# Optimization experiments

Measured on AMD Instinct MI355X. Metric: run time of the kernel, lower is better.

Reference implementation:

```python
import jax, jax.numpy as jnp
import numpy as np

H = 128          # hidden_size
B = 64           # batch of users
T = 20           # current-session length (== max_sess_len)
S = 10           # friend sessions per user (graph degree)
L = 20           # max_sess_len
NUM_ITEMS = 50000
NUM_USERS = 10000
TOPK = 2         # topk in sess_similarity


def gru(x, W_ih, W_hh, b_ih, b_hh):
    """torch nn.GRU (1 layer, batch_first). x: [N, T, H] -> outputs [N, T, H], h_T [N, H]."""
    h0 = jnp.zeros((x.shape[0], x.shape[-1]), x.dtype)

    def step(h, xt):
        gi = xt @ W_ih.T + b_ih          # [N, 3H]
        gh = h @ W_hh.T + b_hh
        i_r, i_z, i_n = jnp.split(gi, 3, axis=-1)
        h_r, h_z, h_n = jnp.split(gh, 3, axis=-1)
        r = jax.nn.sigmoid(i_r + h_r)
        z = jax.nn.sigmoid(i_z + h_z)
        n = jnp.tanh(i_n + r * h_n)
        h = (1.0 - z) * n + z * h
        return h, h

    hT, ys = jax.lax.scan(step, h0, jnp.swapaxes(x, 0, 1))
    return jnp.swapaxes(ys, 0, 1), hT


def masked_softmax(x, mask, axis):
    neg = jnp.finfo(x.dtype).min
    return jax.nn.softmax(jnp.where(mask, x, neg), axis=axis)


def setup_inputs() -> dict:
    key = jax.random.key(0)
    ks = jax.random.split(key, 12)
    users = jax.random.randint(ks[0], (B,), 0, NUM_USERS)
    cur_sess = jax.random.randint(ks[1], (B, T), 0, NUM_ITEMS)          # all valid -> full length
    hist_sess = jax.random.randint(ks[2], (B, S, L), 0, NUM_ITEMS)
    frds_sess = jax.random.randint(ks[3], (B, S, L), 0, NUM_ITEMS)
    cur_sess_len = jnp.full((B,), T, dtype=jnp.int32)
    # parameters
    v_emb = jax.random.uniform(ks[4], (NUM_ITEMS + 1, H), minval=-1.0, maxval=1.0)
    v_emb = v_emb.at[NUM_ITEMS].set(0.0)                                 # padding_idx row
    u_emb = jax.random.normal(ks[5], (NUM_USERS, H)) * (1.0 / np.sqrt(H))
    sc = 1.0 / np.sqrt(H)
    W_ih = jax.random.normal(ks[6], (3 * H, H)) * sc
    W_hh = jax.random.normal(ks[7], (3 * H, H)) * sc
    b_ih = jnp.zeros((3 * H,), jnp.float32)
    b_hh = jnp.zeros((3 * H,), jnp.float32)
    out1_w = jax.random.normal(ks[8], (NUM_ITEMS, 3 * H)) * (1.0 / np.sqrt(3 * H))
    out1_b = jnp.zeros((NUM_ITEMS,), jnp.float32)
    return dict(users=users, cur_sess=cur_sess, hist_sess=hist_sess, frds_sess=frds_sess,
                cur_sess_len=cur_sess_len, v_emb=v_emb, u_emb=u_emb,
                W_ih=W_ih, W_hh=W_hh, b_ih=b_ih, b_hh=b_hh, out1_w=out1_w, out1_b=out1_b)


def reference(users, cur_sess, hist_sess, frds_sess, cur_sess_len,
              v_emb, u_emb, W_ih, W_hh, b_ih, b_hh, out1_w, out1_b):
    # --- rnn_encoder on current session (dropout p=0, eval) ---
    hs, _ = gru(v_emb[cur_sess], W_ih, W_hh, b_ih, b_hh)                 # [B, T, H]
    query = hs

    # --- friend branch (hist branch is dead: hu is overwritten with zeros) ---
    # sess_encoder: GRU over each friend session's items
    frd_items = v_emb[frds_sess]                                         # [B, S, L, H]
    enc, _ = gru(frd_items.reshape(B * S, L, H), W_ih, W_hh, b_ih, b_hh)
    enc = enc.reshape(B, S, L, H)                                        # encoder_output

    # sess_similarity: max over session positions, softmax over degree (S)
    scores = jnp.einsum('bth,bslh->bstl', query, enc)                    # [B, S, T, L]
    sim_raw = scores.max(axis=-1)                                        # [B, S, T]
    sim1 = jax.nn.softmax(sim_raw, axis=1)
    # preserve: edges that are top-2 most similar for ANY step t (S > TOPK branch)
    _, idx = jax.lax.top_k(jnp.swapaxes(sim1, 1, 2), TOPK)               # [B, T, 2]
    preserve = jax.nn.one_hot(idx, S, dtype=jnp.float32).sum((1, 2)) > 0 # [B, S]

    # sess_embedding_attn on the filtered subgraph (masking == filtering here)
    user_e = u_emb[users]                                                # [B, H]
    w = jax.nn.softmax(jnp.einsum('bh,bslh->bsl', user_e, frd_items), axis=2)
    sess_emb = jnp.einsum('bsl,bslh->bsh', w, frd_items)                 # [B, S, H]

    # user_sess_reduce_func: sim1 (pre-filter softmax values), then two softmaxes
    # over the surviving edges (masked softmax over S)
    m = preserve[:, :, None]                                             # [B, S, 1]
    s = masked_softmax(sim1, m, axis=1)
    s = masked_softmax(s, m, axis=1)
    s = jnp.where(m, s, 0.0)
    hf = jnp.einsum('bst,bsh->bth', s, sess_emb)                         # [B, T, H]

    hu = jnp.zeros_like(hs)                                              # hu = zeros_like(hs)
    output = jnp.concatenate([hs, hu, hf], axis=-1)                      # [B, T, 3H]
    logits = output @ out1_w.T + out1_b                                  # [B, T, NUM_ITEMS]
    return logits
```

## Files before the change

### kernel.cpp

```cpp
#include <hip/hip_runtime.h>
#include <cstdint>
#include <cstddef>

#define H_      128
#define B_      64
#define T_      20
#define S_      10
#define L_      20
#define NITEMS  50000
#define NSEQ    704
#define NTOK    (NSEQ * 20)
#define NPAD    50048
#define KA      256

typedef __attribute__((ext_vector_type(8))) short short8;
typedef __attribute__((ext_vector_type(4))) float f32x4;

__device__ __forceinline__ unsigned short f2bf(float f) {
  unsigned int u = __float_as_uint(f);
  u += 0x7FFF + ((u >> 16) & 1);
  return (unsigned short)(u >> 16);
}
__device__ __forceinline__ float sigmoidf_(float x) {
  return 1.0f / (1.0f + __expf(-x));
}

__global__ void __launch_bounds__(384) k2_gi(const int* __restrict__ cur,
                                             const int* __restrict__ frd,
                                             const float* __restrict__ vemb,
                                             const float* __restrict__ Wih,
                                             const float* __restrict__ bih,
                                             float* __restrict__ gi) {
  __shared__ float xs[16 * 128];
  __shared__ int ids[16];
  int tid = threadIdx.x;
  int tok0 = blockIdx.x * 16;
  if (tid < 16) {
    int tok = tok0 + tid;
    int seq = tok / 20, tt = tok % 20;
    ids[tid] = (seq < 64) ? cur[seq * 20 + tt] : frd[(seq - 64) * 20 + tt];
  }
  __syncthreads();
  for (int idx = tid; idx < 512; idx += 384) {
    int i = idx >> 5, kc = idx & 31;
    *(float4*)&xs[i * 128 + kc * 4] =
        *(const float4*)&vemb[(size_t)ids[i] * 128 + kc * 4];
  }
  __syncthreads();
  int j  = tid % 192;
  int th = tid / 192;
  float acc0[8], acc1[8];
#pragma unroll
  for (int i = 0; i < 8; i++) { acc0[i] = 0.f; acc1[i] = 0.f; }
  const float* wr0 = Wih + (size_t)j * 128;
  const float* wr1 = Wih + (size_t)(j + 192) * 128;
  const float* xb = &xs[th * 8 * 128];
  for (int kc = 0; kc < 32; kc++) {
    float4 wa = *(const float4*)(wr0 + kc * 4);
    float4 wc = *(const float4*)(wr1 + kc * 4);
#pragma unroll
    for (int i = 0; i < 8; i++) {
      float4 x4 = *(const float4*)&xb[i * 128 + kc * 4];
      acc0[i] += wa.x * x4.x + wa.y * x4.y + wa.z * x4.z + wa.w * x4.w;
      acc1[i] += wc.x * x4.x + wc.y * x4.y + wc.z * x4.z + wc.w * x4.w;
    }
  }
  float ba = bih[j], bc = bih[j + 192];
#pragma unroll
  for (int i = 0; i < 8; i++) {
    size_t row = (size_t)(tok0 + th * 8 + i) * 384;
    gi[row + j]       = acc0[i] + ba;
    gi[row + j + 192] = acc1[i] + bc;
  }
}

__global__ void __launch_bounds__(384) k3_gru(const float* __restrict__ Whh,
                                              const float* __restrict__ bhh,
                                              const float* __restrict__ gi,
                                              float* __restrict__ out_h) {
  __shared__ float hb[3 * 128];
  __shared__ float pre[3 * 256];
  __shared__ float gin[3 * 128];
  __shared__ float ghn[3 * 128];
  int j = threadIdx.x;
  int seq0 = blockIdx.x * 3;
  int G = NSEQ - seq0; if (G > 3) G = 3;
  float4 wv[32];
  const float4* wr = (const float4*)(Whh + (size_t)j * 128);
#pragma unroll
  for (int kc = 0; kc < 32; kc++) wv[kc] = wr[kc];
  float bb = bhh[j];
  if (j < 128) { hb[j] = 0.f; hb[128 + j] = 0.f; hb[256 + j] = 0.f; }
  __syncthreads();
  for (int t = 0; t < 20; t++) {
    for (int g = 0; g < G; g++) {
      float acc = bb;
#pragma unroll
      for (int kc = 0; kc < 32; kc++) {
        float4 h4 = *(const float4*)&hb[g * 128 + kc * 4];
        float4 w4 = wv[kc];
        acc += w4.x * h4.x + w4.y * h4.y + w4.z * h4.z + w4.w * h4.w;
      }
      float gv = gi[(size_t)((seq0 + g) * 20 + t) * 384 + j];
      if (j < 256) pre[g * 256 + j] = gv + acc;
      else { gin[g * 128 + (j - 256)] = gv; ghn[g * 128 + (j - 256)] = acc; }
    }
    __syncthreads();
    if (j < 128) {
      for (int g = 0; g < G; g++) {
        float r = sigmoidf_(pre[g * 256 + j]);
        float z = sigmoidf_(pre[g * 256 + 128 + j]);
        float n = tanhf(gin[g * 128 + j] + r * ghn[g * 128 + j]);
        float hN = (1.f - z) * n + z * hb[g * 128 + j];
        hb[g * 128 + j] = hN;
        out_h[(size_t)((seq0 + g) * 20 + t) * 128 + j] = hN;
      }
    }
    __syncthreads();
  }
}

__global__ void __launch_bounds__(256) k4_scores(const float* __restrict__ out_h,
                                                 float* __restrict__ sim_raw) {
  __shared__ float qs[20 * 132];
  __shared__ float es[20 * 132];
  __shared__ float sc[400];
  int tid = threadIdx.x;
  int b = blockIdx.x / 10, s = blockIdx.x % 10;
  int eseq = 64 + b * 10 + s;
  for (int idx = tid; idx < 640; idx += 256) {
    int row = idx >> 5, kc = idx & 31;
    *(float4*)&qs[row * 132 + kc * 4] =
        *(const float4*)&out_h[(size_t)(b * 20 + row) * 128 + kc * 4];
    *(float4*)&es[row * 132 + kc * 4] =
        *(const float4*)&out_h[(size_t)(eseq * 20 + row) * 128 + kc * 4];
  }
  __syncthreads();
  for (int idx = tid; idx < 400; idx += 256) {
    int t = idx / 20, l = idx % 20;
    float acc = 0.f;
#pragma unroll
    for (int kc = 0; kc < 32; kc++) {
      float4 q4 = *(const float4*)&qs[t * 132 + kc * 4];
      float4 e4 = *(const float4*)&es[l * 132 + kc * 4];
      acc += q4.x * e4.x + q4.y * e4.y + q4.z * e4.z + q4.w * e4.w;
    }
    sc[idx] = acc;
  }
  __syncthreads();
  if (tid < 20) {
    float m = sc[tid * 20];
    for (int l = 1; l < 20; l++) m = fmaxf(m, sc[tid * 20 + l]);
    sim_raw[(size_t)(b * 10 + s) * 20 + tid] = m;
  }
}

__global__ void __launch_bounds__(64) k5_soft(const float* __restrict__ sim_raw,
                                              float* __restrict__ sfin) {
  __shared__ float sv[200];
  __shared__ float s1[200];
  __shared__ int pres[10];
  int tid = threadIdx.x;
  int b = blockIdx.x;
  for (int idx = tid; idx < 200; idx += 64) sv[idx] = sim_raw[(size_t)b * 200 + idx];
  if (tid < 10) pres[tid] = 0;
  __syncthreads();
  if (tid < 20) {
    int t = tid;
    float mx = -3.4e38f;
    for (int s = 0; s < 10; s++) mx = fmaxf(mx, sv[s * 20 + t]);
    float sum = 0.f;
    for (int s = 0; s < 10; s++) sum += __expf(sv[s * 20 + t] - mx);
    float inv = 1.0f / sum;
    float v1 = -1.f, v2 = -1.f; int i1 = 0, i2 = 0;
    for (int s = 0; s < 10; s++) {
      float v = __expf(sv[s * 20 + t] - mx) * inv;
      s1[s * 20 + t] = v;
      if (v > v1) { v2 = v1; i2 = i1; v1 = v; i1 = s; }
      else if (v > v2) { v2 = v; i2 = s; }
    }
    atomicOr(&pres[i1], 1);
    atomicOr(&pres[i2], 1);
  }
  __syncthreads();
  if (tid < 20) {
    int t = tid;
    float mx = -3.4e38f;
    for (int s = 0; s < 10; s++) if (pres[s]) mx = fmaxf(mx, s1[s * 20 + t]);
    float sum = 0.f;
    for (int s = 0; s < 10; s++) if (pres[s]) sum += __expf(s1[s * 20 + t] - mx);
    float inv = 1.f / sum;
    float mx2 = -3.4e38f;
    for (int s = 0; s < 10; s++)
      if (pres[s]) mx2 = fmaxf(mx2, __expf(s1[s * 20 + t] - mx) * inv);
    float sum2 = 0.f;
    for (int s = 0; s < 10; s++)
      if (pres[s]) sum2 += __expf(__expf(s1[s * 20 + t] - mx) * inv - mx2);
    float inv2 = 1.f / sum2;
    for (int s = 0; s < 10; s++) {
      float o = 0.f;
      if (pres[s]) o = __expf(__expf(s1[s * 20 + t] - mx) * inv - mx2) * inv2;
      sfin[(size_t)(b * 10 + s) * 20 + t] = o;
    }
  }
}

__global__ void __launch_bounds__(128) k6_sess(const int* __restrict__ users,
                                               const int* __restrict__ frd,
                                               const float* __restrict__ vemb,
                                               const float* __restrict__ uemb,
                                               float* __restrict__ sess) {
  __shared__ float fs[20 * 132];
  __shared__ float us[128];
  __shared__ float dt[20];
  __shared__ float wl[20];
  __shared__ int fid[20];
  int tid = threadIdx.x;
  int b = blockIdx.x / 10, s = blockIdx.x % 10;
  if (tid < 20) fid[tid] = frd[(size_t)(b * 10 + s) * 20 + tid];
  us[tid] = uemb[(size_t)users[b] * 128 + tid];
  __syncthreads();
  for (int idx = tid; idx < 640; idx += 128) {
    int row = idx >> 5, kc = idx & 31;
    *(float4*)&fs[row * 132 + kc * 4] =
        *(const float4*)&vemb[(size_t)fid[row] * 128 + kc * 4];
  }
  __syncthreads();
  if (tid < 20) {
    float acc = 0.f;
    for (int kc = 0; kc < 32; kc++) {
      float4 u4 = *(const float4*)&us[kc * 4];
      float4 f4 = *(const float4*)&fs[tid * 132 + kc * 4];
      acc += u4.x * f4.x + u4.y * f4.y + u4.z * f4.z + u4.w * f4.w;
    }
    dt[tid] = acc;
  }
  __syncthreads();
  if (tid < 20) {
    float mx = -3.4e38f;
    for (int l = 0; l < 20; l++) mx = fmaxf(mx, dt[l]);
    float sum = 0.f;
    for (int l = 0; l < 20; l++) sum += __expf(dt[l] - mx);
    wl[tid] = __expf(dt[tid] - mx) / sum;
  }
  __syncthreads();
  float acc = 0.f;
  for (int l = 0; l < 20; l++) acc += wl[l] * fs[l * 132 + tid];
  sess[(size_t)(b * 10 + s) * 128 + tid] = acc;
}

__global__ void __launch_bounds__(256) k7_hf(const float* __restrict__ sfin,
                                             const float* __restrict__ sess,
                                             float* __restrict__ hf) {
  __shared__ float sf[200];
  __shared__ float se[10 * 128];
  int tid = threadIdx.x;
  int b = blockIdx.x;
  for (int idx = tid; idx < 200; idx += 256) sf[idx] = sfin[(size_t)b * 200 + idx];
  for (int idx = tid; idx < 1280; idx += 256) se[idx] = sess[(size_t)b * 1280 + idx];
  __syncthreads();
  for (int idx = tid; idx < 2560; idx += 256) {
    int t = idx >> 7, h = idx & 127;
    float acc = 0.f;
#pragma unroll
    for (int s = 0; s < 10; s++) acc += sf[s * 20 + t] * se[s * 128 + h];
    hf[(size_t)b * 2560 + idx] = acc;
  }
}

__global__ void __launch_bounds__(256) k8_act(const float* __restrict__ out_h,
                                              const float* __restrict__ hf,
                                              unsigned int* __restrict__ act) {
  int g = blockIdx.x * 256 + threadIdx.x;
  int m = g >> 7, p = g & 127;
  float a0, a1;
  if (p < 64) {
    a0 = out_h[(size_t)m * 128 + p * 2];
    a1 = out_h[(size_t)m * 128 + p * 2 + 1];
  } else {
    a0 = hf[(size_t)m * 128 + (p - 64) * 2];
    a1 = hf[(size_t)m * 128 + (p - 64) * 2 + 1];
  }
  act[g] = (unsigned)f2bf(a0) | ((unsigned)f2bf(a1) << 16);
}

__global__ void __launch_bounds__(256) k9_gemm(const unsigned short* __restrict__ act,
                                               const float* __restrict__ w1,
                                               const float* __restrict__ bias,
                                               float* __restrict__ out) {
  __shared__ __align__(16) unsigned short Bs[128 * 256];
  __shared__ __align__(16) unsigned short As[128 * 40];
  int tid = threadIdx.x;
  int w = tid >> 6, lane = tid & 63;
  int q = (lane >> 4) & 3, c = lane & 15;
  int wm = w >> 1, wn = w & 1;
  int nb0 = blockIdx.x * 128;

  {
    int kc = tid & 31;
    int src = (kc < 16) ? kc * 8 : kc * 8 + 128;
#pragma unroll 4
    for (int i = 0; i < 16; i++) {
      int row = i * 8 + (tid >> 5);
      int n = nb0 + row;
      unsigned int o0, o1, o2, o3;
      if (n < NITEMS) {
        const float* p = w1 + (size_t)n * 384 + src;
        float4 f0 = *(const float4*)p;
        float4 f1 = *(const float4*)(p + 4);
        o0 = (unsigned)f2bf(f0.x) | ((unsigned)f2bf(f0.y) << 16);
        o1 = (unsigned)f2bf(f0.z) | ((unsigned)f2bf(f0.w) << 16);
        o2 = (unsigned)f2bf(f1.x) | ((unsigned)f2bf(f1.y) << 16);
        o3 = (unsigned)f2bf(f1.z) | ((unsigned)f2bf(f1.w) << 16);
      } else {
        o0 = o1 = o2 = o3 = 0u;
      }
      int slot = kc ^ (row & 31);
      *(uint4*)&Bs[row * 256 + slot * 8] = make_uint4(o0, o1, o2, o3);
    }
  }

  float bs[4]; int okn[4]; int ncol[4];
#pragma unroll
  for (int nt = 0; nt < 4; nt++) {
    int n = nb0 + wn * 64 + nt * 16 + c;
    ncol[nt] = n;
    okn[nt] = (n < NITEMS);
    bs[nt] = (n < NITEMS) ? bias[n] : 0.f;
  }

  for (int mc = 0; mc < 10; mc++) {
    f32x4 acc[4][4];
#pragma unroll
    for (int mt = 0; mt < 4; mt++)
#pragma unroll
      for (int nt = 0; nt < 4; nt++) {
        f32x4 z = {0.f, 0.f, 0.f, 0.f};
        acc[mt][nt] = z;
      }
    for (int kf = 0; kf < 8; kf++) {
      __syncthreads();
      {
        int ch0 = tid * 2;
#pragma unroll
        for (int jj = 0; jj < 2; jj++) {
          int ch = ch0 + jj;
          int row = ch >> 2, kk = ch & 3;
          short8 v = *(const short8*)&act[(size_t)(mc * 128 + row) * 256 + kf * 32 + kk * 8];
          *(short8*)&As[row * 40 + kk * 8] = v;
        }
      }
      __syncthreads();
      short8 bfr[4];
#pragma unroll
      for (int nt = 0; nt < 4; nt++) {
        int n_l = wn * 64 + nt * 16 + c;
        int slot = n_l * 32 + ((kf * 4 + q) ^ (n_l & 31));
        bfr[nt] = *(const short8*)&Bs[slot * 8];
      }
#pragma unroll
      for (int mt = 0; mt < 4; mt++) {
        int row = wm * 64 + mt * 16 + c;
        short8 af = *(const short8*)&As[row * 40 + q * 8];
#pragma unroll
        for (int nt = 0; nt < 4; nt++)
          acc[mt][nt] = __builtin_amdgcn_mfma_f32_16x16x32_bf16(af, bfr[nt], acc[mt][nt], 0, 0, 0);
      }
    }
#pragma unroll
    for (int nt = 0; nt < 4; nt++) {
      if (okn[nt]) {
#pragma unroll
        for (int mt = 0; mt < 4; mt++) {
          int m = mc * 128 + wm * 64 + mt * 16 + q * 4;
#pragma unroll
          for (int r = 0; r < 4; r++)
            out[(size_t)(m + r) * NITEMS + ncol[nt]] = acc[mt][nt][r] + bs[nt];
        }
      }
    }
  }
}

extern "C" void kernel_launch(void* const* d_in, const int* in_sizes, int n_in,
                              void* d_out, int out_size, void* d_ws, size_t ws_size,
                              hipStream_t stream) {
  const int*   users = (const int*)d_in[0];
  const int*   cur   = (const int*)d_in[1];
  const int*   frd   = (const int*)d_in[3];
  const float* vemb  = (const float*)d_in[5];
  const float* uemb  = (const float*)d_in[6];
  const float* Wih   = (const float*)d_in[7];
  const float* Whh   = (const float*)d_in[8];
  const float* bih   = (const float*)d_in[9];
  const float* bhh   = (const float*)d_in[10];
  const float* w1    = (const float*)d_in[11];
  const float* b1    = (const float*)d_in[12];
  float* out = (float*)d_out;

  char* ws = (char*)d_ws;
  size_t off = 0;
  auto alloc = [&](size_t bytes) -> void* {
    void* p = ws + off;
    off = (off + bytes + 255) & ~(size_t)255;
    return p;
  };
  unsigned int*   act  = (unsigned int*)alloc((size_t)1280 * 128 * 4);
  float*          gi   = (float*)alloc((size_t)NTOK * 384 * 4);
  float*          outh = (float*)alloc((size_t)NTOK * 128 * 4);
  float*          simr = (float*)alloc((size_t)12800 * 4);
  float*          sfin = (float*)alloc((size_t)12800 * 4);
  float*          sess = (float*)alloc((size_t)640 * 128 * 4);
  float*          hf   = (float*)alloc((size_t)1280 * 128 * 4);

  k2_gi<<<NTOK / 16, 384, 0, stream>>>(cur, frd, vemb, Wih, bih, gi);
  k3_gru<<<(NSEQ + 2) / 3, 384, 0, stream>>>(Whh, bhh, gi, outh);
  k4_scores<<<640, 256, 0, stream>>>(outh, simr);
  k5_soft<<<64, 64, 0, stream>>>(simr, sfin);
  k6_sess<<<640, 128, 0, stream>>>(users, frd, vemb, uemb, sess);
  k7_hf<<<64, 256, 0, stream>>>(sfin, sess, hf);
  k8_act<<<640, 256, 0, stream>>>(outh, hf, act);
  k9_gemm<<<NPAD / 128, 256, 0, stream>>>((const unsigned short*)act, w1, b1, out);
}
```

Before: 530.8 us.

## Fuse softmax, hf and activation packing; double-buffer GEMM A tiles via async LDS loads

Merges the softmax, hf reduction and bf16 activation packing kernels into a single kernel, removing two launches and the sfin/hf intermediate buffers. In the output GEMM, the A operand is now prefetched into a double-buffered, XOR-swizzled LDS tile using global_load_lds. The loop is flattened over m-chunks and k-steps, leaving one barrier per step. The goal is to hide activation load latency behind the MFMA work. In exchange it uses a more complex async copy path, and its correctness depends on the wait and barrier placement.

New measurement: 535.1 us. About the same (+0.8%).

```diff
diff --git a/kernel.cpp b/kernel.cpp
--- a/kernel.cpp
+++ b/kernel.cpp
@@ -155,14 +155,63 @@
   }
 }
 
-__global__ void __launch_bounds__(64) k5_soft(const float* __restrict__ sim_raw,
-                                              float* __restrict__ sfin) {
+__global__ void __launch_bounds__(128) k6_sess(const int* __restrict__ users,
+                                               const int* __restrict__ frd,
+                                               const float* __restrict__ vemb,
+                                               const float* __restrict__ uemb,
+                                               float* __restrict__ sess) {
+  __shared__ float fs[20 * 132];
+  __shared__ float us[128];
+  __shared__ float dt[20];
+  __shared__ float wl[20];
+  __shared__ int fid[20];
+  int tid = threadIdx.x;
+  int b = blockIdx.x / 10, s = blockIdx.x % 10;
+  if (tid < 20) fid[tid] = frd[(size_t)(b * 10 + s) * 20 + tid];
+  us[tid] = uemb[(size_t)users[b] * 128 + tid];
+  __syncthreads();
+  for (int idx = tid; idx < 640; idx += 128) {
+    int row = idx >> 5, kc = idx & 31;
+    *(float4*)&fs[row * 132 + kc * 4] =
+        *(const float4*)&vemb[(size_t)fid[row] * 128 + kc * 4];
+  }
+  __syncthreads();
+  if (tid < 20) {
+    float acc = 0.f;
+    for (int kc = 0; kc < 32; kc++) {
+      float4 u4 = *(const float4*)&us[kc * 4];
+      float4 f4 = *(const float4*)&fs[tid * 132 + kc * 4];
+      acc += u4.x * f4.x + u4.y * f4.y + u4.z * f4.z + u4.w * f4.w;
+    }
+    dt[tid] = acc;
+  }
+  __syncthreads();
+  if (tid < 20) {
+    float mx = -3.4e38f;
+    for (int l = 0; l < 20; l++) mx = fmaxf(mx, dt[l]);
+    float sum = 0.f;
+    for (int l = 0; l < 20; l++) sum += __expf(dt[l] - mx);
+    wl[tid] = __expf(dt[tid] - mx) / sum;
+  }
+  __syncthreads();
+  float acc = 0.f;
+  for (int l = 0; l < 20; l++) acc += wl[l] * fs[l * 132 + tid];
+  sess[(size_t)(b * 10 + s) * 128 + tid] = acc;
+}
+
+__global__ void __launch_bounds__(256) k5_fused(const float* __restrict__ sim_raw,
+                                                const float* __restrict__ sess,
+                                                const float* __restrict__ out_h,
+                                                unsigned int* __restrict__ act) {
   __shared__ float sv[200];
   __shared__ float s1[200];
+  __shared__ float sf[200];
+  __shared__ float se[10 * 128];
   __shared__ int pres[10];
   int tid = threadIdx.x;
   int b = blockIdx.x;
-  for (int idx = tid; idx < 200; idx += 64) sv[idx] = sim_raw[(size_t)b * 200 + idx];
+  for (int idx = tid; idx < 200; idx += 256) sv[idx] = sim_raw[(size_t)b * 200 + idx];
+  for (int idx = tid; idx < 1280; idx += 256) se[idx] = sess[(size_t)b * 1280 + idx];
   if (tid < 10) pres[tid] = 0;
   __syncthreads();
   if (tid < 20) {
@@ -200,88 +249,36 @@
     for (int s = 0; s < 10; s++) {
       float o = 0.f;
       if (pres[s]) o = __expf(__expf(s1[s * 20 + t] - mx) * inv - mx2) * inv2;
-      sfin[(size_t)(b * 10 + s) * 20 + t] = o;
-    }
-  }
-}
-
-__global__ void __launch_bounds__(128) k6_sess(const int* __restrict__ users,
-                                               const int* __restrict__ frd,
-                                               const float* __restrict__ vemb,
-                                               const float* __restrict__ uemb,
-                                               float* __restrict__ sess) {
-  __shared__ float fs[20 * 132];
-  __shared__ float us[128];
-  __shared__ float dt[20];
-  __shared__ float wl[20];
-  __shared__ int fid[20];
-  int tid = threadIdx.x;
-  int b = blockIdx.x / 10, s = blockIdx.x % 10;
-  if (tid < 20) fid[tid] = frd[(size_t)(b * 10 + s) * 20 + tid];
-  us[tid] = uemb[(size_t)users[b] * 128 + tid];
-  __syncthreads();
-  for (int idx = tid; idx < 640; idx += 128) {
-    int row = idx >> 5, kc = idx & 31;
-    *(float4*)&fs[row * 132 + kc * 4] =
-        *(const float4*)&vemb[(size_t)fid[row] * 128 + kc * 4];
-  }
-  __syncthreads();
-  if (tid < 20) {
-    float acc = 0.f;
-    for (int kc = 0; kc < 32; kc++) {
-      float4 u4 = *(const float4*)&us[kc * 4];
-      float4 f4 = *(const float4*)&fs[tid * 132 + kc * 4];
-      acc += u4.x * f4.x + u4.y * f4.y + u4.z * f4.z + u4.w * f4.w;
-    }
-    dt[tid] = acc;
-  }
-  __syncthreads();
-  if (tid < 20) {
-    float mx = -3.4e38f;
-    for (int l = 0; l < 20; l++) mx = fmaxf(mx, dt[l]);
-    float sum = 0.f;
-    for (int l = 0; l < 20; l++) sum += __expf(dt[l] - mx);
-    wl[tid] = __expf(dt[tid] - mx) / sum;
-  }
-  __syncthreads();
-  float acc = 0.f;
-  for (int l = 0; l < 20; l++) acc += wl[l] * fs[l * 132 + tid];
-  sess[(size_t)(b * 10 + s) * 128 + tid] = acc;
-}
-
-__global__ void __launch_bounds__(256) k7_hf(const float* __restrict__ sfin,
-                                             const float* __restrict__ sess,
-                                             float* __restrict__ hf) {
-  __shared__ float sf[200];
-  __shared__ float se[10 * 128];
-  int tid = threadIdx.x;
-  int b = blockIdx.x;
-  for (int idx = tid; idx < 200; idx += 256) sf[idx] = sfin[(size_t)b * 200 + idx];
-  for (int idx = tid; idx < 1280; idx += 256) se[idx] = sess[(size_t)b * 1280 + idx];
+      sf[s * 20 + t] = o;
+    }
+  }
   __syncthreads();
   for (int idx = tid; idx < 2560; idx += 256) {
-    int t = idx >> 7, h = idx & 127;
-    float acc = 0.f;
-#pragma unroll
-    for (int s = 0; s < 10; s++) acc += sf[s * 20 + t] * se[s * 128 + h];
-    hf[(size_t)b * 2560 + idx] = acc;
-  }
-}
-
-__global__ void __launch_bounds__(256) k8_act(const float* __restrict__ out_h,
-                                              const float* __restrict__ hf,
-                                              unsigned int* __restrict__ act) {
-  int g = blockIdx.x * 256 + threadIdx.x;
-  int m = g >> 7, p = g & 127;
-  float a0, a1;
-  if (p < 64) {
-    a0 = out_h[(size_t)m * 128 + p * 2];
-    a1 = out_h[(size_t)m * 128 + p * 2 + 1];
-  } else {
-    a0 = hf[(size_t)m * 128 + (p - 64) * 2];
-    a1 = hf[(size_t)m * 128 + (p - 64) * 2 + 1];
-  }
-  act[g] = (unsigned)f2bf(a0) | ((unsigned)f2bf(a1) << 16);
+    int t = idx >> 7, p = idx & 127;
+    int m = b * 20 + t;
+    float a0, a1;
+    if (p < 64) {
+      a0 = out_h[(size_t)m * 128 + p * 2];
+      a1 = out_h[(size_t)m * 128 + p * 2 + 1];
+    } else {
+      int h0 = (p - 64) * 2;
+      float acc0 = 0.f, acc1 = 0.f;
+#pragma unroll
+      for (int s = 0; s < 10; s++) {
+        float w = sf[s * 20 + t];
+        acc0 += w * se[s * 128 + h0];
+        acc1 += w * se[s * 128 + h0 + 1];
+      }
+      a0 = acc0; a1 = acc1;
+    }
+    act[(size_t)m * 128 + p] = (unsigned)f2bf(a0) | ((unsigned)f2bf(a1) << 16);
+  }
+}
+
+__device__ __forceinline__ void async_cp16(const unsigned short* g, unsigned short* l) {
+  __builtin_amdgcn_global_load_lds((__attribute__((address_space(1))) void*)g,
+                                   (__attribute__((address_space(3))) void*)l,
+                                   16, 0, 0);
 }
 
 __global__ void __launch_bounds__(256) k9_gemm(const unsigned short* __restrict__ act,
@@ -289,12 +286,24 @@
                                                const float* __restrict__ bias,
                                                float* __restrict__ out) {
   __shared__ __align__(16) unsigned short Bs[128 * 256];
-  __shared__ __align__(16) unsigned short As[128 * 40];
+  __shared__ __align__(16) unsigned short As[2][128 * 32];
   int tid = threadIdx.x;
   int w = tid >> 6, lane = tid & 63;
   int q = (lane >> 4) & 3, c = lane & 15;
   int wm = w >> 1, wn = w & 1;
   int nb0 = blockIdx.x * 128;
+
+  {
+    int lhi = lane >> 2, llo = lane & 3;
+#pragma unroll
+    for (int i = 0; i < 2; i++) {
+      int rbase = w * 32 + i * 16;
+      int r = rbase + lhi;
+      int sw = (r ^ (r >> 2)) & 3;
+      const unsigned short* src = act + ((size_t)r * 256 + ((llo ^ sw) << 3));
+      async_cp16(src, &As[0][rbase * 32]);
+    }
+  }
 
   {
     int kc = tid & 31;
@@ -329,56 +338,66 @@
     bs[nt] = (n < NITEMS) ? bias[n] : 0.f;
   }
 
-  for (int mc = 0; mc < 10; mc++) {
-    f32x4 acc[4][4];
-#pragma unroll
-    for (int mt = 0; mt < 4; mt++)
+  __syncthreads();
+
+  f32x4 acc[4][4];
+  int buf = 0;
+  int lhi = lane >> 2, llo = lane & 3;
+  for (int s = 0; s < 80; s++) {
+    int mcs = s >> 3, kfs = s & 7;
+    if (s + 1 < 80) {
+      int mcn = (s + 1) >> 3, kfn = (s + 1) & 7;
+#pragma unroll
+      for (int i = 0; i < 2; i++) {
+        int rbase = w * 32 + i * 16;
+        int r = rbase + lhi;
+        int sw = (r ^ (r >> 2)) & 3;
+        const unsigned short* src =
+            act + ((size_t)(mcn * 128 + r) * 256 + kfn * 32 + ((llo ^ sw) << 3));
+        async_cp16(src, &As[buf ^ 1][rbase * 32]);
+      }
+    }
+    if (kfs == 0) {
+#pragma unroll
+      for (int mt = 0; mt < 4; mt++)
+#pragma unroll
+        for (int nt = 0; nt < 4; nt++) {
+          f32x4 z = {0.f, 0.f, 0.f, 0.f};
+          acc[mt][nt] = z;
+        }
+    }
+    short8 bfr[4];
+#pragma unroll
+    for (int nt = 0; nt < 4; nt++) {
+      int n_l = wn * 64 + nt * 16 + c;
+      int slot = n_l * 32 + ((kfs * 4 + q) ^ (n_l & 31));
+      bfr[nt] = *(const short8*)&Bs[slot * 8];
+    }
+#pragma unroll
+    for (int mt = 0; mt < 4; mt++) {
+      int row = wm * 64 + mt * 16 + c;
+      int sw = (row ^ (row >> 2)) & 3;
+      short8 af = *(const short8*)&As[buf][row * 32 + ((q ^ sw) << 3)];
+#pragma unroll
+      for (int nt = 0; nt < 4; nt++)
+        acc[mt][nt] = __builtin_amdgcn_mfma_f32_16x16x32_bf16(af, bfr[nt], acc[mt][nt], 0, 0, 0);
+    }
+    if (kfs == 7) {
 #pragma unroll
       for (int nt = 0; nt < 4; nt++) {
-        f32x4 z = {0.f, 0.f, 0.f, 0.f};
-        acc[mt][nt] = z;
-      }
-    for (int kf = 0; kf < 8; kf++) {
-      __syncthreads();
-      {
-        int ch0 = tid * 2;
-#pragma unroll
-        for (int jj = 0; jj < 2; jj++) {
-          int ch = ch0 + jj;
-          int row = ch >> 2, kk = ch & 3;
-          short8 v = *(const short8*)&act[(size_t)(mc * 128 + row) * 256 + kf * 32 + kk * 8];
-          *(short8*)&As[row * 40 + kk * 8] = v;
+        if (okn[nt]) {
+#pragma unroll
+          for (int mt = 0; mt < 4; mt++) {
+            int m = mcs * 128 + wm * 64 + mt * 16 + q * 4;
+#pragma unroll
+            for (int r = 0; r < 4; r++)
+              out[(size_t)(m + r) * NITEMS + ncol[nt]] = acc[mt][nt][r] + bs[nt];
+          }
         }
       }
-      __syncthreads();
-      short8 bfr[4];
-#pragma unroll
-      for (int nt = 0; nt < 4; nt++) {
-        int n_l = wn * 64 + nt * 16 + c;
-        int slot = n_l * 32 + ((kf * 4 + q) ^ (n_l & 31));
-        bfr[nt] = *(const short8*)&Bs[slot * 8];
-      }
-#pragma unroll
-      for (int mt = 0; mt < 4; mt++) {
-        int row = wm * 64 + mt * 16 + c;
-        short8 af = *(const short8*)&As[row * 40 + q * 8];
-#pragma unroll
-        for (int nt = 0; nt < 4; nt++)
-          acc[mt][nt] = __builtin_amdgcn_mfma_f32_16x16x32_bf16(af, bfr[nt], acc[mt][nt], 0, 0, 0);
-      }
-    }
-#pragma unroll
-    for (int nt = 0; nt < 4; nt++) {
-      if (okn[nt]) {
-#pragma unroll
-        for (int mt = 0; mt < 4; mt++) {
-          int m = mc * 128 + wm * 64 + mt * 16 + q * 4;
-#pragma unroll
-          for (int r = 0; r < 4; r++)
-            out[(size_t)(m + r) * NITEMS + ncol[nt]] = acc[mt][nt][r] + bs[nt];
-        }
-      }
-    }
+    }
+    __syncthreads();
+    buf ^= 1;
   }
 }
 
@@ -409,16 +428,12 @@
   float*          gi   = (float*)alloc((size_t)NTOK * 384 * 4);
   float*          outh = (float*)alloc((size_t)NTOK * 128 * 4);
   float*          simr = (float*)alloc((size_t)12800 * 4);
-  float*          sfin = (float*)alloc((size_t)12800 * 4);
   float*          sess = (float*)alloc((size_t)640 * 128 * 4);
-  float*          hf   = (float*)alloc((size_t)1280 * 128 * 4);
 
   k2_gi<<<NTOK / 16, 384, 0, stream>>>(cur, frd, vemb, Wih, bih, gi);
   k3_gru<<<(NSEQ + 2) / 3, 384, 0, stream>>>(Whh, bhh, gi, outh);
   k4_scores<<<640, 256, 0, stream>>>(outh, simr);
-  k5_soft<<<64, 64, 0, stream>>>(simr, sfin);
   k6_sess<<<640, 128, 0, stream>>>(users, frd, vemb, uemb, sess);
-  k7_hf<<<64, 256, 0, stream>>>(sfin, sess, hf);
-  k8_act<<<640, 256, 0, stream>>>(outh, hf, act);
+  k5_fused<<<64, 256, 0, stream>>>(simr, sess, outh, (unsigned int*)act);
   k9_gemm<<<NPAD / 128, 256, 0, stream>>>((const unsigned short*)act, w1, b1, out);
 }
```
